# Optimization experiments

Measured on AMD Instinct MI355X. Metric: run time of the kernel, lower is better.

Reference implementation:

```python
import jax, jax.numpy as jnp
import numpy as np
import math

D_MODEL = 1024
NUM_HEADS = 16
D_K = D_MODEL // NUM_HEADS
D_FF = 4096
NUM_LAYERS = 6  # NOTE: the torch Encoder reuses the SAME EncoderLayer object, so weights are shared
LN_EPS = 1e-5


def _layernorm(x, scale, bias):
    mu = jnp.mean(x, axis=-1, keepdims=True)
    var = jnp.var(x, axis=-1, keepdims=True)
    return (x - mu) * jax.lax.rsqrt(var + LN_EPS) * scale + bias


def setup_inputs() -> dict:
    key = jax.random.key(0)
    ks = jax.random.split(key, 16)
    s = 0.02
    inp = {
        "x": jax.random.normal(ks[0], (2, 2048, D_MODEL), dtype=jnp.float32),
        "mask": jnp.ones((2, 1, 1, 2048), dtype=bool),
        "wq": jax.random.normal(ks[1], (D_MODEL, D_MODEL), jnp.float32) * s,
        "bq": jnp.zeros((D_MODEL,), jnp.float32),
        "wk": jax.random.normal(ks[2], (D_MODEL, D_MODEL), jnp.float32) * s,
        "bk": jnp.zeros((D_MODEL,), jnp.float32),
        "wv": jax.random.normal(ks[3], (D_MODEL, D_MODEL), jnp.float32) * s,
        "bv": jnp.zeros((D_MODEL,), jnp.float32),
        "wo": jax.random.normal(ks[4], (D_MODEL, D_MODEL), jnp.float32) * s,
        "bo": jnp.zeros((D_MODEL,), jnp.float32),
        "w1": jax.random.normal(ks[5], (D_MODEL, D_FF), jnp.float32) * s,
        "b1": jnp.zeros((D_FF,), jnp.float32),
        "w2": jax.random.normal(ks[6], (D_FF, D_MODEL), jnp.float32) * s,
        "b2": jnp.zeros((D_MODEL,), jnp.float32),
        "ln1_s": jnp.ones((D_MODEL,), jnp.float32),
        "ln1_b": jnp.zeros((D_MODEL,), jnp.float32),
        "ln2_s": jnp.ones((D_MODEL,), jnp.float32),
        "ln2_b": jnp.zeros((D_MODEL,), jnp.float32),
        "lnf_s": jnp.ones((D_MODEL,), jnp.float32),
        "lnf_b": jnp.zeros((D_MODEL,), jnp.float32),
    }
    return inp


def _attention(xn, mask, wq, bq, wk, bk, wv, bv, wo, bo):
    B, S, _ = xn.shape
    q = (xn @ wq + bq).reshape(B, S, NUM_HEADS, D_K).transpose(0, 2, 1, 3)
    k = (xn @ wk + bk).reshape(B, S, NUM_HEADS, D_K).transpose(0, 2, 1, 3)
    v = (xn @ wv + bv).reshape(B, S, NUM_HEADS, D_K).transpose(0, 2, 1, 3)
    scores = jnp.einsum("bhqd,bhkd->bhqk", q, k) / math.sqrt(D_K)  # [B,H,S,S]
    scores = jnp.where(mask, scores, jnp.float32(-1e9))
    attn = jax.nn.softmax(scores, axis=-1)
    out = jnp.einsum("bhqk,bhkd->bhqd", attn, v)
    out = out.transpose(0, 2, 1, 3).reshape(B, S, D_MODEL)
    return out @ wo + bo


def reference(x, mask, wq, bq, wk, bk, wv, bv, wo, bo, w1, b1, w2, b2,
              ln1_s, ln1_b, ln2_s, ln2_b, lnf_s, lnf_b):
    h = x
    for _ in range(NUM_LAYERS):  # shared weights across layers (faithful to source)
        # pre-LN self-attention sublayer with residual
        h = h + _attention(_layernorm(h, ln1_s, ln1_b), mask,
                           wq, bq, wk, bk, wv, bv, wo, bo)
        # pre-LN FFN sublayer with residual
        hn = _layernorm(h, ln2_s, ln2_b)
        h = h + (jax.nn.relu(hn @ w1 + b1) @ w2 + b2)
    return _layernorm(h, lnf_s, lnf_b)
```

## Files before the change

kernel.cpp:

```cpp
#include <hip/hip_runtime.h>
#include <stdint.h>


#define S_LEN 2048
#define NTOK 4096
#define MBYTE (1u << 20)

typedef __attribute__((ext_vector_type(8))) short bf16x8;
typedef __attribute__((ext_vector_type(4))) short bf16x4;
typedef __attribute__((ext_vector_type(4))) float f32x4;
typedef __attribute__((ext_vector_type(16))) float f32x16;
typedef __attribute__((ext_vector_type(4))) int i32x4;

#define MFMA16 __builtin_amdgcn_mfma_f32_16x16x32_bf16
#define MFMA32 __builtin_amdgcn_mfma_f32_32x32x16_bf16

#define S_BARRIER __builtin_amdgcn_s_barrier()
#define SCHED_FENCE __builtin_amdgcn_sched_barrier(0)
#define LGKM0 asm volatile("s_waitcnt lgkmcnt(0)" ::: "memory")
#define VMCNT(n) asm volatile("s_waitcnt vmcnt(" #n ")" ::: "memory")

static __device__ __forceinline__ short f2bf(float f) {
    union { float f; uint32_t u; } a; a.f = f;
    uint32_t r = a.u + 0x7FFFu + ((a.u >> 16) & 1u);
    return (short)(r >> 16);
}

static __device__ __forceinline__ void gload_lds16(const void* g, void* l) {
    __builtin_amdgcn_global_load_lds(
        (const __attribute__((address_space(1))) void*)g,
        (__attribute__((address_space(3))) void*)l, 16, 0, 0);
}

__global__ __launch_bounds__(256)
void transpose_cast(const float* __restrict__ in, short* __restrict__ out,
                    int R, int C)
{
    __shared__ float tile[64][65];
    const int t  = threadIdx.x;
    const int bc = blockIdx.x * 64;
    const int br = blockIdx.y * 64;
    const int rl = t >> 2;
    const int c0 = (t & 3) * 16;
    const float* src = in + (size_t)(br + rl) * C + bc + c0;
#pragma unroll
    for (int i = 0; i < 4; ++i) {
        f32x4 v = *(const f32x4*)(src + i * 4);
        tile[rl][c0 + i*4 + 0] = v[0];
        tile[rl][c0 + i*4 + 1] = v[1];
        tile[rl][c0 + i*4 + 2] = v[2];
        tile[rl][c0 + i*4 + 3] = v[3];
    }
    __syncthreads();
    const int cl = t >> 2;
    const int r0 = (t & 3) * 16;
    bf16x8 o0, o1;
#pragma unroll
    for (int j = 0; j < 8; ++j) o0[j] = f2bf(tile[r0 + j][cl]);
#pragma unroll
    for (int j = 0; j < 8; ++j) o1[j] = f2bf(tile[r0 + 8 + j][cl]);
    short* dst = out + (size_t)(bc + cl) * R + br + r0;
    *(bf16x8*)dst       = o0;
    *(bf16x8*)(dst + 8) = o1;
}

__global__ void concat_bias(const float* __restrict__ bq, const float* __restrict__ bk,
                            const float* __restrict__ bv, float* __restrict__ o)
{
    int i = blockIdx.x * 256 + threadIdx.x;
    o[i] = (i < 1024) ? bq[i] : (i < 2048) ? bk[i - 1024] : bv[i - 2048];
}

template<int OUT_F32>
__global__ __launch_bounds__(256)
void ln_kernel(const float* __restrict__ x, const float* __restrict__ sc,
               const float* __restrict__ bi, void* __restrict__ outp)
{
    const int row = blockIdx.x;
    const int t = threadIdx.x;
    const float* xr = x + (size_t)row * 1024;
    f32x4 v = *(const f32x4*)(xr + t * 4);
    float sum = v[0] + v[1] + v[2] + v[3];
    float sq  = v[0]*v[0] + v[1]*v[1] + v[2]*v[2] + v[3]*v[3];
#pragma unroll
    for (int m = 1; m <= 32; m <<= 1) {
        sum += __shfl_xor(sum, m);
        sq  += __shfl_xor(sq, m);
    }
    __shared__ float rs[4], rq[4];
    const int w = t >> 6;
    if ((t & 63) == 0) { rs[w] = sum; rq[w] = sq; }
    __syncthreads();
    sum = rs[0] + rs[1] + rs[2] + rs[3];
    sq  = rq[0] + rq[1] + rq[2] + rq[3];
    const float mu   = sum * (1.0f / 1024.0f);
    const float var  = sq * (1.0f / 1024.0f) - mu * mu;
    const float rstd = rsqrtf(var + 1e-5f);
    f32x4 s4 = *(const f32x4*)(sc + t * 4);
    f32x4 b4 = *(const f32x4*)(bi + t * 4);
    f32x4 o;
#pragma unroll
    for (int j = 0; j < 4; ++j) o[j] = (v[j] - mu) * rstd * s4[j] + b4[j];
    if (OUT_F32) {
        *(f32x4*)((float*)outp + (size_t)row * 1024 + t * 4) = o;
    } else {
        bf16x4 ob;
#pragma unroll
        for (int j = 0; j < 4; ++j) ob[j] = f2bf(o[j]);
        *(bf16x4*)((short*)outp + (size_t)row * 1024 + t * 4) = ob;
    }
}

template<int MODE>
__global__ __launch_bounds__(512, 2)
void gemm256(const short* __restrict__ A, const short* __restrict__ Bt,
             const float* __restrict__ bias, short* __restrict__ Cout,
             int M, int N, int K)
{
    __shared__ __align__(16) char SM[139264];
    const int t = threadIdx.x;
    const int w = t >> 6, l = t & 63;
    const int lr = l & 15, lk = l >> 4;
    const int wm = w >> 2, wn = w & 3;

    const int gx = gridDim.x;
    const int nwg = gx * gridDim.y;
    int id = blockIdx.y * gx + blockIdx.x;
    {
        const int q = nwg >> 3, r = nwg & 7;
        const int xcd = id & 7, idx = id >> 3;
        id = (xcd < r ? xcd * (q + 1) : r * (q + 1) + (xcd - r) * q) + idx;
    }
    const int bn = (id % gx) * 256;
    const int bm = (id / gx) * 256;

    f32x4 acc[8][4];
#pragma unroll
    for (int i = 0; i < 8; ++i)
#pragma unroll
        for (int j = 0; j < 4; ++j) acc[i][j] = (f32x4)0.0f;

    const int rowt = t >> 3;
    const int kc   = (t & 7) ^ (rowt & 7);
    const short* gA = A  + (size_t)(bm + rowt) * K + kc * 8;
    const short* gB = Bt + (size_t)(bn + rowt) * K + kc * 8;

#define ABASE(b, hh) (SM + (b) * 65536 + (hh) * 16384)
#define BBASE(b, hh) (SM + (b) * 65536 + 32768 + (hh) * 16384)

    auto stg = [&](const short* g, char* hbase, int hh, int T) {
        const short* s = g + (size_t)(hh * 128) * K + T * 64;
        gload_lds16(s,                  hbase + t * 16);
        gload_lds16(s + (size_t)64 * K, hbase + 8192 + t * 16);
    };

    const int par = lr & 7;
    const int bhh = wn >> 1;
    bf16x8 bfr[4][2], af[2][2];

#define READ_B(buf) do {                                                     \
    const char* BB = BBASE(buf, bhh);                                        \
    _Pragma("unroll") for (int jn = 0; jn < 4; ++jn)                         \
      _Pragma("unroll") for (int kk = 0; kk < 2; ++kk)                       \
        bfr[jn][kk] = *(const bf16x8*)(BB + ((wn & 1) * 64 + jn * 16 + lr)   \
                       * 128 + (((kk * 4 + lk) ^ par) << 4));                \
} while (0)

#define READ_A(buf, q) do {                                                  \
    const char* AB = ABASE(buf, wm);                                         \
    _Pragma("unroll") for (int ii = 0; ii < 2; ++ii)                         \
      _Pragma("unroll") for (int kk = 0; kk < 2; ++kk)                       \
        af[ii][kk] = *(const bf16x8*)(AB + (((q) * 2 + ii) * 16 + lr) * 128  \
                       + (((kk * 4 + lk) ^ par) << 4));                      \
} while (0)

#define MM(q) do {                                                           \
    __builtin_amdgcn_s_setprio(1);                                           \
    _Pragma("unroll") for (int ii = 0; ii < 2; ++ii)                         \
      _Pragma("unroll") for (int jn = 0; jn < 4; ++jn) {                     \
        acc[(q)*2+ii][jn] = MFMA16(af[ii][0], bfr[jn][0], acc[(q)*2+ii][jn], 0,0,0); \
        acc[(q)*2+ii][jn] = MFMA16(af[ii][1], bfr[jn][1], acc[(q)*2+ii][jn], 0,0,0); \
      }                                                                      \
    __builtin_amdgcn_s_setprio(0);                                           \
} while (0)

    const int nk = K >> 6;
    const int ni = nk >> 1;

    stg(gA, ABASE(0, 0), 0, 0); stg(gA, ABASE(0, 1), 1, 0);
    stg(gB, BBASE(0, 0), 0, 0); stg(gB, BBASE(0, 1), 1, 0);
    stg(gB, BBASE(1, 0), 0, 1); stg(gB, BBASE(1, 1), 1, 1);
    VMCNT(4);
    S_BARRIER;

    for (int i = 0; i < ni - 1; ++i) {
        const int T1 = 2 * i + 1;
        READ_B(0); READ_A(0, 0); stg(gA, ABASE(1, 0), 0, T1);
        SCHED_FENCE; S_BARRIER; LGKM0; SCHED_FENCE; MM(0); S_BARRIER;
        READ_A(0, 1); stg(gA, ABASE(1, 1), 1, T1);
        SCHED_FENCE; S_BARRIER; LGKM0; SCHED_FENCE; MM(1); S_BARRIER;
        READ_A(0, 2); stg(gB, BBASE(0, 0), 0, T1 + 1);
        SCHED_FENCE; S_BARRIER; LGKM0; SCHED_FENCE; MM(2); S_BARRIER;
        READ_A(0, 3); stg(gB, BBASE(0, 1), 1, T1 + 1);
        SCHED_FENCE; S_BARRIER; LGKM0; SCHED_FENCE; MM(3); VMCNT(4); S_BARRIER;
        READ_B(1); READ_A(1, 0); stg(gA, ABASE(0, 0), 0, T1 + 1);
        SCHED_FENCE; S_BARRIER; LGKM0; SCHED_FENCE; MM(0); S_BARRIER;
        READ_A(1, 1); stg(gA, ABASE(0, 1), 1, T1 + 1);
        SCHED_FENCE; S_BARRIER; LGKM0; SCHED_FENCE; MM(1); S_BARRIER;
        READ_A(1, 2); stg(gB, BBASE(1, 0), 0, T1 + 2);
        SCHED_FENCE; S_BARRIER; LGKM0; SCHED_FENCE; MM(2); S_BARRIER;
        READ_A(1, 3); stg(gB, BBASE(1, 1), 1, T1 + 2);
        SCHED_FENCE; S_BARRIER; LGKM0; SCHED_FENCE; MM(3); VMCNT(4); S_BARRIER;
    }
    {
        READ_B(0); READ_A(0, 0); stg(gA, ABASE(1, 0), 0, nk - 1);
        SCHED_FENCE; S_BARRIER; LGKM0; SCHED_FENCE; MM(0); S_BARRIER;
        READ_A(0, 1); stg(gA, ABASE(1, 1), 1, nk - 1);
        SCHED_FENCE; S_BARRIER; LGKM0; SCHED_FENCE; MM(1); S_BARRIER;
        READ_A(0, 2);
        SCHED_FENCE; S_BARRIER; LGKM0; SCHED_FENCE; MM(2); S_BARRIER;
        READ_A(0, 3);
        SCHED_FENCE; S_BARRIER; LGKM0; SCHED_FENCE; MM(3); VMCNT(0); S_BARRIER;
        READ_B(1); READ_A(1, 0);
        SCHED_FENCE; S_BARRIER; LGKM0; SCHED_FENCE; MM(0); S_BARRIER;
        READ_A(1, 1);
        SCHED_FENCE; S_BARRIER; LGKM0; SCHED_FENCE; MM(1); S_BARRIER;
        READ_A(1, 2);
        SCHED_FENCE; S_BARRIER; LGKM0; SCHED_FENCE; MM(2); S_BARRIER;
        READ_A(1, 3);
        SCHED_FENCE; S_BARRIER; LGKM0; SCHED_FENCE; MM(3); S_BARRIER;
    }

    char* ep = SM + w * 17408;
#pragma unroll
    for (int jn = 0; jn < 4; ++jn) {
        const int col = bn + wn * 64 + jn * 16 + lr;
        const float bv = bias[col];
        const float qscale = (MODE == 3 && col < 1024) ? 0.1803368801f : 1.0f;
#pragma unroll
        for (int i = 0; i < 8; ++i) {
#pragma unroll
            for (int r = 0; r < 4; ++r) {
                float v = acc[i][jn][r] + bv;
                if (MODE == 1) v = fmaxf(v, 0.0f);
                if (MODE == 3) v *= qscale;
                *(short*)(ep + (i * 16 + lk * 4 + r) * 136
                             + (jn * 16 + lr) * 2) = f2bf(v);
            }
        }
    }
    LGKM0; SCHED_FENCE;
#pragma unroll
    for (int e = 0; e < 16; ++e) {
        const int row = e * 8 + (l >> 3);
        i32x4 vv = *(const i32x4*)(ep + row * 136 + (l & 7) * 16);
        *(i32x4*)(Cout + (size_t)(bm + wm * 128 + row) * N
                       + bn + wn * 64 + (l & 7) * 8) = vv;
    }
#undef READ_B
#undef READ_A
#undef MM
#undef ABASE
#undef BBASE
}

template<int MODE>
__global__ __launch_bounds__(512, 4)
void gemm_bt(const short* __restrict__ A, const short* __restrict__ Bt,
             const float* __restrict__ bias, const float* __restrict__ res,
             void* __restrict__ Cout, int M, int N, int K)
{
    __shared__ __align__(16) short As[2][128 * 32];
    __shared__ __align__(16) short Bs[2][128 * 32];
    const int t = threadIdx.x;
    const int w = t >> 6, l = t & 63;
    const int lr = l & 15, lk = l >> 4;

    const int gx = gridDim.x;
    const int nwg = gx * gridDim.y;
    int id = blockIdx.y * gx + blockIdx.x;
    {
        const int q = nwg >> 3, r = nwg & 7;
        const int xcd = id & 7, idx = id >> 3;
        id = (xcd < r ? xcd * (q + 1) : r * (q + 1) + (xcd - r) * q) + idx;
    }
    const int bn = (id % gx) * 128;
    const int bm = (id / gx) * 128;
    const int wr = (w >> 1) * 32, wc = (w & 1) * 64;

    f32x4 acc[2][4];
#pragma unroll
    for (int i = 0; i < 2; ++i)
#pragma unroll
        for (int j = 0; j < 4; ++j) acc[i][j] = (f32x4)0.0f;

    const short* gA0 = A  + (size_t)(bm + (t >> 2)) * K + (t & 3) * 8;
    const short* gB0 = Bt + (size_t)(bn + (t >> 2)) * K + (t & 3) * 8;

    i32x4 q0[2], q1[2], q2[2], q3[2];

    auto LOADT = [&](i32x4 (&r)[2], int k0) {
        r[0] = *(const i32x4*)(gA0 + k0);
        r[1] = *(const i32x4*)(gB0 + k0);
    };
    auto WRITET = [&](int buf, const i32x4 (&r)[2]) {
        *(i32x4*)((char*)As[buf] + t * 16) = r[0];
        *(i32x4*)((char*)Bs[buf] + t * 16) = r[1];
    };
    auto COMPUTE = [&](int buf) {
        const short* Ab = As[buf];
        const short* Bb = Bs[buf];
        bf16x8 af[2], bfr[4];
#pragma unroll
        for (int i = 0; i < 2; ++i)
            af[i] = *(const bf16x8*)(Ab + (wr + i * 16 + lr) * 32 + lk * 8);
#pragma unroll
        for (int j = 0; j < 4; ++j)
            bfr[j] = *(const bf16x8*)(Bb + (wc + j * 16 + lr) * 32 + lk * 8);
#pragma unroll
        for (int i = 0; i < 2; ++i)
#pragma unroll
            for (int j = 0; j < 4; ++j)
                acc[i][j] = MFMA16(af[i], bfr[j], acc[i][j], 0, 0, 0);
    };

    const int nk = K >> 5;
    LOADT(q0, 0);
    LOADT(q1, 32);
    LOADT(q2, 64);
    LOADT(q3, 96);
    WRITET(0, q0);
    LGKM0;
    S_BARRIER;

    for (int s = 0; s < nk; s += 4) {
        WRITET(1, q1);
        if (s + 4 < nk) LOADT(q0, (s + 4) * 32);
        COMPUTE(0);
        LGKM0; S_BARRIER;
        WRITET(0, q2);
        if (s + 5 < nk) LOADT(q1, (s + 5) * 32);
        COMPUTE(1);
        LGKM0; S_BARRIER;
        WRITET(1, q3);
        if (s + 6 < nk) LOADT(q2, (s + 6) * 32);
        COMPUTE(0);
        LGKM0; S_BARRIER;
        if (s + 4 < nk) WRITET(0, q0);
        if (s + 7 < nk) LOADT(q3, (s + 7) * 32);
        COMPUTE(1);
        LGKM0; S_BARRIER;
    }

#pragma unroll
    for (int j = 0; j < 4; ++j) {
        const int col = bn + wc + j * 16 + lr;
        const float bv = bias[col];
#pragma unroll
        for (int i = 0; i < 2; ++i) {
            const int row0 = bm + wr + i * 16 + lk * 4;
#pragma unroll
            for (int r = 0; r < 4; ++r) {
                const int row = row0 + r;
                float v = acc[i][j][r] + bv;
                if (MODE == 1) v = fmaxf(v, 0.0f);
                if (MODE == 2) {
                    float* C = (float*)Cout;
                    C[(size_t)row * N + col] = v + res[(size_t)row * N + col];
                } else {
                    short* C = (short*)Cout;
                    C[(size_t)row * N + col] = f2bf(v);
                }
            }
        }
    }
}

__global__ __launch_bounds__(256)
void v_transpose(const short* __restrict__ qkv, short* __restrict__ vT)
{
    __shared__ short tile[64][72];
    const int bh = blockIdx.x;
    const int sblk = blockIdx.y;
    const int b = bh >> 4, h = bh & 15;
    const int t = threadIdx.x;
    const int sl = t >> 2;
    const int d0 = (t & 3) * 16;
    const short* src = qkv + (size_t)(b * S_LEN + sblk * 64 + sl) * 3072 + 2048 + h * 64 + d0;
    bf16x8 a = *(const bf16x8*)src;
    bf16x8 c = *(const bf16x8*)(src + 8);
#pragma unroll
    for (int j = 0; j < 8; ++j) { tile[sl][d0 + j] = a[j]; tile[sl][d0 + 8 + j] = c[j]; }
    __syncthreads();
    const int dl = t >> 2;
    const int s0 = (t & 3) * 16;
    bf16x8 o0, o1;
#pragma unroll
    for (int j = 0; j < 8; ++j) o0[j] = tile[s0 + j][dl];
#pragma unroll
    for (int j = 0; j < 8; ++j) o1[j] = tile[s0 + 8 + j][dl];
    short* dst = vT + (size_t)(bh * 64 + dl) * S_LEN + sblk * 64 + s0;
    *(bf16x8*)dst       = o0;
    *(bf16x8*)(dst + 8) = o1;
}

__global__ __launch_bounds__(256, 2)
void attn_fwd(const short* __restrict__ qkv, const short* __restrict__ vT,
              short* __restrict__ outp)
{
    __shared__ __align__(16) char Kt[2][8192];
    __shared__ __align__(16) char Vt[2][8192];

    const int bh = blockIdx.x;
    const int qblk = blockIdx.y;
    const int b = bh >> 4, h = bh & 15;
    const int t = threadIdx.x;
    const int w = t >> 6, l = t & 63;
    const int l31 = l & 31, lh = l >> 5;
    const int q0 = qblk * 128 + w * 32;

    const short* qp = qkv + (size_t)(b * S_LEN + q0 + l31) * 3072 + h * 64 + lh * 8;
    bf16x8 aq[4];
#pragma unroll
    for (int kh = 0; kh < 4; ++kh)
        aq[kh] = *(const bf16x8*)(qp + kh * 16);

    const int r0  = t >> 3;
    const int sc0 = (t & 7) ^ (r0 & 7);
    const short* kst = qkv + (size_t)(b * S_LEN + r0) * 3072 + 1024 + h * 64 + sc0 * 8;
    const short* vst = vT + (size_t)bh * 64 * S_LEN + (size_t)r0 * S_LEN + sc0 * 8;
    const int dst0 = w * 1024;
    const int dst1 = 4096 + w * 1024;

    int offs[4];
#pragma unroll
    for (int x = 0; x < 4; ++x)
        offs[x] = l31 * 128 + (((2 * x + lh) ^ (l31 & 7)) << 4);

    f32x16 acc0 = (f32x16)0.0f, acc1 = (f32x16)0.0f;
    float lsum = 0.0f;

    gload_lds16(kst,                Kt[0] + dst0);
    gload_lds16(kst + 32 * 3072,    Kt[0] + dst1);
    gload_lds16(vst,                Vt[0] + dst0);
    gload_lds16(vst + 32 * S_LEN,   Vt[0] + dst1);

    int cur = 0;
    for (int tt = 0; tt < 32; ++tt) {
        __syncthreads();
        if (tt + 1 < 32) {
            const short* kn = kst + (size_t)(tt + 1) * 64 * 3072;
            const short* vn = vst + (tt + 1) * 64;
            gload_lds16(kn,              Kt[cur ^ 1] + dst0);
            gload_lds16(kn + 32 * 3072,  Kt[cur ^ 1] + dst1);
            gload_lds16(vn,              Vt[cur ^ 1] + dst0);
            gload_lds16(vn + 32 * S_LEN, Vt[cur ^ 1] + dst1);
        }
        const char* K = Kt[cur];
        const char* V = Vt[cur];

#pragma unroll
        for (int jb = 0; jb < 2; ++jb) {
            f32x16 st = (f32x16)0.0f;
#pragma unroll
            for (int kh = 0; kh < 4; ++kh) {
                bf16x8 kf = *(const bf16x8*)(K + jb * 4096 + offs[kh]);
                st = MFMA32(kf, aq[kh], st, 0, 0, 0);
            }
            uint32_t wd[8];
#pragma unroll
            for (int m = 0; m < 8; ++m) {
                float pa = __builtin_amdgcn_exp2f(st[2 * m]);
                float pb = __builtin_amdgcn_exp2f(st[2 * m + 1]);
                lsum += pa + pb;
                asm("v_cvt_pk_bf16_f32 %0, %1, %2" : "=v"(wd[m]) : "v"(pa), "v"(pb));
            }
#pragma unroll
            for (int ksl = 0; ksl < 2; ++ksl) {
                uint32_t x0 = wd[4 * ksl + 2], y0 = wd[4 * ksl];
                uint32_t x1 = wd[4 * ksl + 3], y1 = wd[4 * ksl + 1];
                asm("v_permlane32_swap_b32 %0, %1" : "+v"(x0), "+v"(y0));
                asm("v_permlane32_swap_b32 %0, %1" : "+v"(x1), "+v"(y1));
                union { uint32_t u[4]; bf16x8 v; } fr;
                fr.u[0] = y0; fr.u[1] = y1; fr.u[2] = x0; fr.u[3] = x1;
                const int ks = jb * 2 + ksl;
                bf16x8 vf0 = *(const bf16x8*)(V + offs[ks]);
                bf16x8 vf1 = *(const bf16x8*)(V + 4096 + offs[ks]);
                acc0 = MFMA32(vf0, fr.v, acc0, 0, 0, 0);
                acc1 = MFMA32(vf1, fr.v, acc1, 0, 0, 0);
            }
        }
        cur ^= 1;
    }

    lsum += __shfl_xor(lsum, 32);
    const float inv = 1.0f / lsum;

    const size_t orow = (size_t)(b * S_LEN + q0 + l31) * 1024 + h * 64;
#pragma unroll
    for (int reg = 0; reg < 16; ++reg) {
        const int dl = (reg & 3) + 8 * (reg >> 2) + 4 * lh;
        outp[orow + dl]      = f2bf(acc0[reg] * inv);
        outp[orow + 32 + dl] = f2bf(acc1[reg] * inv);
    }
}

extern "C" void kernel_launch(void* const* d_in, const int* in_sizes, int n_in,
                              void* d_out, int out_size, void* d_ws, size_t ws_size,
                              hipStream_t stream)
{
    const float* x     = (const float*)d_in[0];
    const float* wq    = (const float*)d_in[2];
    const float* bq    = (const float*)d_in[3];
    const float* wk    = (const float*)d_in[4];
    const float* bk    = (const float*)d_in[5];
    const float* wv    = (const float*)d_in[6];
    const float* bv    = (const float*)d_in[7];
    const float* wo    = (const float*)d_in[8];
    const float* bo    = (const float*)d_in[9];
    const float* w1    = (const float*)d_in[10];
    const float* b1    = (const float*)d_in[11];
    const float* w2    = (const float*)d_in[12];
    const float* b2    = (const float*)d_in[13];
    const float* ln1_s = (const float*)d_in[14];
    const float* ln1_b = (const float*)d_in[15];
    const float* ln2_s = (const float*)d_in[16];
    const float* ln2_b = (const float*)d_in[17];
    const float* lnf_s = (const float*)d_in[18];
    const float* lnf_b = (const float*)d_in[19];

    char* ws = (char*)d_ws;
    if (ws_size < (size_t)89 * MBYTE) return;

    float* h     = (float*)(ws);
    short* xn    = (short*)(ws + (size_t)16 * MBYTE);
    short* qkvb  = (short*)(ws + (size_t)24 * MBYTE);
    short* vT    = (short*)(ws + (size_t)48 * MBYTE);
    short* aout  = (short*)(ws + (size_t)56 * MBYTE);
    short* ffh   = (short*)(ws + (size_t)24 * MBYTE);
    short* wqkvT = (short*)(ws + (size_t)64 * MBYTE);
    short* woT   = (short*)(ws + (size_t)70 * MBYTE);
    short* w1T   = (short*)(ws + (size_t)72 * MBYTE);
    short* w2T   = (short*)(ws + (size_t)80 * MBYTE);
    float* bqkv  = (float*)(ws + (size_t)88 * MBYTE);

    transpose_cast<<<dim3(16, 16), 256, 0, stream>>>(wq, wqkvT,               1024, 1024);
    transpose_cast<<<dim3(16, 16), 256, 0, stream>>>(wk, wqkvT + 1024 * 1024, 1024, 1024);
    transpose_cast<<<dim3(16, 16), 256, 0, stream>>>(wv, wqkvT + 2048 * 1024, 1024, 1024);
    transpose_cast<<<dim3(16, 16), 256, 0, stream>>>(wo, woT,                 1024, 1024);
    transpose_cast<<<dim3(64, 16), 256, 0, stream>>>(w1, w1T, 1024, 4096);
    transpose_cast<<<dim3(16, 64), 256, 0, stream>>>(w2, w2T, 4096, 1024);
    concat_bias<<<12, 256, 0, stream>>>(bq, bk, bv, bqkv);
    hipMemcpyAsync(h, x, (size_t)NTOK * 1024 * 4, hipMemcpyDeviceToDevice, stream);

    for (int layer = 0; layer < 6; ++layer) {
        ln_kernel<0><<<NTOK, 256, 0, stream>>>(h, ln1_s, ln1_b, xn);
        gemm256<3><<<dim3(12, 16), 512, 0, stream>>>(xn, wqkvT, bqkv, qkvb,
                                                     NTOK, 3072, 1024);
        v_transpose<<<dim3(32, 32), 256, 0, stream>>>(qkvb, vT);
        attn_fwd<<<dim3(32, 16), 256, 0, stream>>>(qkvb, vT, aout);
        gemm_bt<2><<<dim3(8, 32), 512, 0, stream>>>(aout, woT, bo, h, h,
                                                    NTOK, 1024, 1024);
        ln_kernel<0><<<NTOK, 256, 0, stream>>>(h, ln2_s, ln2_b, xn);
        gemm256<1><<<dim3(16, 16), 512, 0, stream>>>(xn, w1T, b1, ffh,
                                                     NTOK, 4096, 1024);
        gemm_bt<2><<<dim3(8, 32), 512, 0, stream>>>(ffh, w2T, b2, h, h,
                                                    NTOK, 1024, 4096);
    }
    ln_kernel<1><<<NTOK, 256, 0, stream>>>(h, lnf_s, lnf_b, d_out);
}
```

Before: 1.229 ms.

## Split-K the output GEMMs and fuse residual reduction into LayerNorm

The Wo and W2 projections now run as two-way split-K GEMMs (grid z=2), each writing a bf16 partial sum, which doubles the workgroup count for these N=1024 GEMMs. The following LayerNorm kernel adds both partials plus bias into the fp32 residual, writes h back, and normalizes. This removes the separate residual read-modify-write epilogue and raises occupancy. The cost is extra partial-buffer traffic and bf16 rounding of the partial sums before they reach the fp32 residual, which may affect accuracy.

Measured after the change: 1.234 ms. No clear change (+0.4%).

```diff
diff --git a/kernel.cpp b/kernel.cpp
--- a/kernel.cpp
+++ b/kernel.cpp
@@ -24,6 +24,11 @@
     union { float f; uint32_t u; } a; a.f = f;
     uint32_t r = a.u + 0x7FFFu + ((a.u >> 16) & 1u);
     return (short)(r >> 16);
+}
+static __device__ __forceinline__ float bf2f(short s) {
+    union { uint32_t u; float f; } a;
+    a.u = ((uint32_t)(uint16_t)s) << 16;
+    return a.f;
 }
 
 static __device__ __forceinline__ void gload_lds16(const void* g, void* l) {
@@ -71,15 +76,28 @@
     o[i] = (i < 1024) ? bq[i] : (i < 2048) ? bk[i - 1024] : bv[i - 2048];
 }
 
-template<int OUT_F32>
+template<int OUT_F32, int HAS_P>
 __global__ __launch_bounds__(256)
-void ln_kernel(const float* __restrict__ x, const float* __restrict__ sc,
-               const float* __restrict__ bi, void* __restrict__ outp)
+void ln_kernel(float* __restrict__ h,
+               const short* __restrict__ P0, const short* __restrict__ P1,
+               const float* __restrict__ gb,
+               const float* __restrict__ sc, const float* __restrict__ bi,
+               void* __restrict__ outp)
 {
     const int row = blockIdx.x;
     const int t = threadIdx.x;
-    const float* xr = x + (size_t)row * 1024;
-    f32x4 v = *(const f32x4*)(xr + t * 4);
+    float* hr = h + (size_t)row * 1024;
+    f32x4 v = *(const f32x4*)(hr + t * 4);
+    if (HAS_P) {
+        bf16x4 p0 = *(const bf16x4*)(P0 + (size_t)row * 1024 + t * 4);
+        bf16x4 p1 = *(const bf16x4*)(P1 + (size_t)row * 1024 + t * 4);
+        f32x4 g4 = *(const f32x4*)(gb + t * 4);
+#pragma unroll
+        for (int j = 0; j < 4; ++j)
+            v[j] += bf2f(p0[j]) + bf2f(p1[j]) + g4[j];
+        if (!OUT_F32)
+            *(f32x4*)(hr + t * 4) = v;
+    }
     float sum = v[0] + v[1] + v[2] + v[3];
     float sq  = v[0]*v[0] + v[1]*v[1] + v[2]*v[2] + v[3]*v[3];
 #pragma unroll
@@ -268,7 +286,8 @@
 __global__ __launch_bounds__(512, 4)
 void gemm_bt(const short* __restrict__ A, const short* __restrict__ Bt,
              const float* __restrict__ bias, const float* __restrict__ res,
-             void* __restrict__ Cout, int M, int N, int K)
+             void* __restrict__ Cout, void* __restrict__ CoutB,
+             int M, int N, int K, int Kstride)
 {
     __shared__ __align__(16) short As[2][128 * 32];
     __shared__ __align__(16) short Bs[2][128 * 32];
@@ -287,6 +306,7 @@
     const int bn = (id % gx) * 128;
     const int bm = (id / gx) * 128;
     const int wr = (w >> 1) * 32, wc = (w & 1) * 64;
+    const int kz = (MODE == 4) ? blockIdx.z * K : 0;
 
     f32x4 acc[2][4];
 #pragma unroll
@@ -294,8 +314,8 @@
 #pragma unroll
         for (int j = 0; j < 4; ++j) acc[i][j] = (f32x4)0.0f;
 
-    const short* gA0 = A  + (size_t)(bm + (t >> 2)) * K + (t & 3) * 8;
-    const short* gB0 = Bt + (size_t)(bn + (t >> 2)) * K + (t & 3) * 8;
+    const short* gA0 = A  + (size_t)(bm + (t >> 2)) * Kstride + (t & 3) * 8 + kz;
+    const short* gB0 = Bt + (size_t)(bn + (t >> 2)) * Kstride + (t & 3) * 8 + kz;
 
     i32x4 q0[2], q1[2], q2[2], q3[2];
 
@@ -352,10 +372,11 @@
         LGKM0; S_BARRIER;
     }
 
+    short* Cp = (short*)((MODE == 4 && blockIdx.z) ? CoutB : Cout);
 #pragma unroll
     for (int j = 0; j < 4; ++j) {
         const int col = bn + wc + j * 16 + lr;
-        const float bv = bias[col];
+        const float bv = (MODE == 4) ? 0.0f : bias[col];
 #pragma unroll
         for (int i = 0; i < 2; ++i) {
             const int row0 = bm + wr + i * 16 + lk * 4;
@@ -368,8 +389,7 @@
                     float* C = (float*)Cout;
                     C[(size_t)row * N + col] = v + res[(size_t)row * N + col];
                 } else {
-                    short* C = (short*)Cout;
-                    C[(size_t)row * N + col] = f2bf(v);
+                    Cp[(size_t)row * N + col] = f2bf(v);
                 }
             }
         }
@@ -538,6 +558,10 @@
     short* vT    = (short*)(ws + (size_t)48 * MBYTE);
     short* aout  = (short*)(ws + (size_t)56 * MBYTE);
     short* ffh   = (short*)(ws + (size_t)24 * MBYTE);
+    short* woP0  = (short*)(ws + (size_t)24 * MBYTE);
+    short* woP1  = (short*)(ws + (size_t)32 * MBYTE);
+    short* w2P0  = xn;
+    short* w2P1  = aout;
     short* wqkvT = (short*)(ws + (size_t)64 * MBYTE);
     short* woT   = (short*)(ws + (size_t)70 * MBYTE);
     short* w1T   = (short*)(ws + (size_t)72 * MBYTE);
@@ -553,19 +577,29 @@
     concat_bias<<<12, 256, 0, stream>>>(bq, bk, bv, bqkv);
     hipMemcpyAsync(h, x, (size_t)NTOK * 1024 * 4, hipMemcpyDeviceToDevice, stream);
 
+    ln_kernel<0, 0><<<NTOK, 256, 0, stream>>>(h, nullptr, nullptr, nullptr,
+                                              ln1_s, ln1_b, xn);
     for (int layer = 0; layer < 6; ++layer) {
-        ln_kernel<0><<<NTOK, 256, 0, stream>>>(h, ln1_s, ln1_b, xn);
         gemm256<3><<<dim3(12, 16), 512, 0, stream>>>(xn, wqkvT, bqkv, qkvb,
                                                      NTOK, 3072, 1024);
         v_transpose<<<dim3(32, 32), 256, 0, stream>>>(qkvb, vT);
         attn_fwd<<<dim3(32, 16), 256, 0, stream>>>(qkvb, vT, aout);
-        gemm_bt<2><<<dim3(8, 32), 512, 0, stream>>>(aout, woT, bo, h, h,
-                                                    NTOK, 1024, 1024);
-        ln_kernel<0><<<NTOK, 256, 0, stream>>>(h, ln2_s, ln2_b, xn);
+        gemm_bt<4><<<dim3(8, 32, 2), 512, 0, stream>>>(aout, woT, nullptr, nullptr,
+                                                       woP0, woP1,
+                                                       NTOK, 1024, 512, 1024);
+        ln_kernel<0, 1><<<NTOK, 256, 0, stream>>>(h, woP0, woP1, bo,
+                                                  ln2_s, ln2_b, xn);
         gemm256<1><<<dim3(16, 16), 512, 0, stream>>>(xn, w1T, b1, ffh,
                                                      NTOK, 4096, 1024);
-        gemm_bt<2><<<dim3(8, 32), 512, 0, stream>>>(ffh, w2T, b2, h, h,
-                                                    NTOK, 1024, 4096);
-    }
-    ln_kernel<1><<<NTOK, 256, 0, stream>>>(h, lnf_s, lnf_b, d_out);
-}
+        gemm_bt<4><<<dim3(8, 32, 2), 512, 0, stream>>>(ffh, w2T, nullptr, nullptr,
+                                                       w2P0, w2P1,
+                                                       NTOK, 1024, 2048, 4096);
+        if (layer < 5) {
+            ln_kernel<0, 1><<<NTOK, 256, 0, stream>>>(h, w2P0, w2P1, b2,
+                                                      ln1_s, ln1_b, xn);
+        } else {
+            ln_kernel<1, 1><<<NTOK, 256, 0, stream>>>(h, w2P0, w2P1, b2,
+                                                      lnf_s, lnf_b, d_out);
+        }
+    }
+}
```
